# Kernel optimization log

Measured on AMD Instinct MI355X. Metric: run time of the kernel, lower is better.

The kernel has to match this reference:

```python
import math
import jax, jax.numpy as jnp
import numpy as np

MUL = 8      # multiplicity of 0e and 1o in irreps_in/out
KS = 5       # kernel spatial extent (diameter 5, steps 1 -> coords -2..2)
NB = 5       # num_radial_basis
RAD = 2.5    # diameter / 2


def _sus(t):
    # e3nn sus(x) = exp(-1/x) for x>0 else 0
    return jnp.where(t > 0.0, jnp.exp(-1.0 / jnp.where(t > 0.0, t, 1.0)), 0.0)


def _emb_sh():
    c = jnp.arange(-2.0, 3.0)
    lat = jnp.stack(jnp.meshgrid(c, c, c, indexing='ij'), axis=-1)  # (5,5,5,3)
    d = jnp.linalg.norm(lat, axis=-1)
    # soft_one_hot_linspace(basis='smooth_finite', cutoff=True)
    values = jnp.linspace(0.0, RAD, NB + 2)
    step = values[1] - values[0]
    diff = (d[..., None] - values[1:-1]) / step
    emb = 1.14136 * math.exp(2.0) * _sus(diff + 1.0) * _sus(1.0 - diff)  # (5,5,5,NB)
    # real spherical harmonics, lmax=2, normalize=True, normalization='component'
    safe = jnp.where(d > 0.0, d, 1.0)[..., None]
    u = jnp.where(d[..., None] > 0.0, lat / safe, 0.0)
    x, y, z = u[..., 0], u[..., 1], u[..., 2]
    s3, s5, s15 = math.sqrt(3.0), math.sqrt(5.0), math.sqrt(15.0)
    sh = jnp.stack([
        jnp.ones_like(x),
        s3 * x, s3 * y, s3 * z,
        s15 * x * z, s15 * x * y,
        s5 * (y * y - 0.5 * (x * x + z * z)),
        s15 * y * z, (s15 / 2.0) * (z * z - x * x),
    ], axis=-1)  # (5,5,5,9)
    return emb, sh


def _c121():
    # Clebsch-Gordan (w3j) for 1o x 2e -> 1o in the real e3nn basis, built from the
    # orthonormal symmetric-traceless matrix basis matching the l=2 SH component order.
    s2, s6 = math.sqrt(2.0), math.sqrt(6.0)
    S = np.zeros((5, 3, 3))
    S[0, 0, 2] = S[0, 2, 0] = 1.0 / s2            # xz
    S[1, 0, 1] = S[1, 1, 0] = 1.0 / s2            # xy
    S[2] = np.diag([-1.0, 2.0, -1.0]) / s6        # 2y^2 - x^2 - z^2
    S[3, 1, 2] = S[3, 2, 1] = 1.0 / s2            # yz
    S[4] = np.diag([-1.0, 0.0, 1.0]) / s2         # z^2 - x^2
    # w3j(1,2,1)[m,j,k] = S[j,m,k]/sqrt(5)  (fully symmetric since l1+l2+l3 even)
    return jnp.asarray(np.transpose(S, (1, 0, 2)) / math.sqrt(5.0), dtype=jnp.float32)


def _build_kernel(weight, emb, sh, c121, dtype):
    g = (KS, KS, KS)
    W = (emb @ weight) / float(KS * KS * KS)  # (5,5,5,320)
    w1, w2, w3, w4, w5 = [W[..., 64 * i:64 * (i + 1)].reshape(g + (MUL, MUL)) for i in range(5)]
    sh0, sh1, sh2 = sh[..., 0], sh[..., 1:4], sh[..., 4:9]
    pw0 = math.sqrt(1.0 / 16.0)   # output 0e: alpha=1, fan_in=8+8
    pw1 = math.sqrt(3.0 / 24.0)   # output 1o: alpha=3, fan_in=8+8+8
    inv_s3 = 1.0 / math.sqrt(3.0)
    K00 = pw0 * sh0[..., None, None] * w1                                   # (g,u,w)
    K01 = (pw1 * inv_s3) * jnp.einsum('xyzuw,xyzk->xyzuwk', w2, sh1)        # (g,u,w,k)
    K10 = (pw0 * inv_s3) * jnp.einsum('xyzuw,xyzm->xyzumw', w4, sh1)        # (g,u,m,w)
    T = jnp.einsum('xyzj,mjk->xyzmk', sh2, c121)                            # (g,m,k)
    eye3 = jnp.eye(3, dtype=dtype)
    K11 = pw1 * (inv_s3 * jnp.einsum('xyzuw,mk->xyzumwk', sh0[..., None, None] * w3, eye3)
                 + jnp.einsum('xyzuw,xyzmk->xyzumwk', w5, T))               # (g,u,m,w,k)
    D = 4 * MUL
    kern = jnp.zeros(g + (D, D), dtype=dtype)
    kern = kern.at[..., :MUL, :MUL].set(K00)
    kern = kern.at[..., :MUL, MUL:].set(K01.reshape(g + (MUL, 3 * MUL)))
    kern = kern.at[..., MUL:, :MUL].set(K10.reshape(g + (3 * MUL, MUL)))
    kern = kern.at[..., MUL:, MUL:].set(K11.reshape(g + (3 * MUL, 3 * MUL)))
    return jnp.transpose(kern, (4, 3, 0, 1, 2))  # 'xyzio->oixyz'


def reference(x, weight, w_sc0, w_sc1):
    emb, sh = _emb_sh()
    c121 = _c121()
    kern = _build_kernel(weight, emb, sh, c121, x.dtype)
    B, _, X, Y, Z = x.shape
    inv_s8 = 1.0 / math.sqrt(MUL)
    # self-connection: e3nn Linear, 0e->0e and 1o->1o blocks
    x0 = x[:, :MUL]
    x1 = x[:, MUL:].reshape(B, MUL, 3, X, Y, Z)
    sc0 = inv_s8 * jnp.einsum('uv,buxyz->bvxyz', w_sc0, x0)
    sc1 = inv_s8 * jnp.einsum('uv,bumxyz->bvmxyz', w_sc1, x1).reshape(B, 3 * MUL, X, Y, Z)
    sc = jnp.concatenate([sc0, sc1], axis=1)
    conv = jax.lax.conv_general_dilated(
        x, kern, window_strides=(1, 1, 1), padding=[(2, 2)] * 3,
        dimension_numbers=('NCDHW', 'OIDHW', 'NCDHW'))
    return sc + conv


def setup_inputs() -> dict:
    key = jax.random.key(0)
    k1, k2, k3, k4 = jax.random.split(key, 4)
    return {
        'x': jax.random.normal(k1, (2, 32, 64, 64, 64), dtype=jnp.float32),
        'weight': jax.random.normal(k2, (NB, 5 * MUL * MUL), dtype=jnp.float32),
        'w_sc0': jax.random.normal(k3, (MUL, MUL), dtype=jnp.float32),
        'w_sc1': jax.random.normal(k4, (MUL, MUL), dtype=jnp.float32),
    }
```

## Files before the change

### kernel.cpp

```cpp
#include <hip/hip_runtime.h>
#include <math.h>

typedef __attribute__((ext_vector_type(8))) short short8;
typedef __attribute__((ext_vector_type(4))) float f32x4;
typedef __attribute__((ext_vector_type(16))) float f32x16;

#define NTAP 125
#define DCH 32

static __device__ __forceinline__ unsigned short f2bf(float f) {
    union { float f; unsigned u; } v; v.f = f;
    unsigned u = v.u;
    return (unsigned short)((u + 0x7FFFu + ((u >> 16) & 1u)) >> 16);
}

static __device__ __forceinline__ void gld_lds16(const void* g, void* l) {
    __builtin_amdgcn_global_load_lds(
        (const __attribute__((address_space(1))) unsigned int*)g,
        (__attribute__((address_space(3))) unsigned int*)l, 16, 0, 0);
}

__global__ __launch_bounds__(128) void build_pack(
    const float* __restrict__ weight,
    const float* __restrict__ w_sc0,
    const float* __restrict__ w_sc1,
    unsigned short* __restrict__ kwb,
    float4* __restrict__ zpg)
{
    const int t = blockIdx.x;
    if (t == 0) {
        float4 z4 = make_float4(0.f, 0.f, 0.f, 0.f);
        zpg[threadIdx.x * 2] = z4;
        zpg[threadIdx.x * 2 + 1] = z4;
    }
    const int dx = t / 25, dy = (t / 5) % 5, dz = t % 5;
    const float px = dx - 2.0f, py = dy - 2.0f, pz = dz - 2.0f;
    const float d = sqrtf(px * px + py * py + pz * pz);

    const float stepv = 2.5f / 6.0f;
    const float embc = 1.14136f * expf(2.0f);
    float emb[5];
#pragma unroll
    for (int n = 0; n < 5; ++n) {
        float diff = (d - stepv * (float)(n + 1)) / stepv;
        float a = diff + 1.0f, bb = 1.0f - diff;
        float v = 0.0f;
        if (a > 0.0f && bb > 0.0f)
            v = embc * expf(-1.0f / a) * expf(-1.0f / bb);
        emb[n] = v;
    }

    const float inv_d = (d > 0.0f) ? 1.0f / d : 0.0f;
    const float ux = px * inv_d, uy = py * inv_d, uz = pz * inv_d;
    const float s3 = 1.73205081f, s5 = 2.23606798f, s15 = 3.87298335f;
    float sh[9];
    sh[0] = 1.0f;
    sh[1] = s3 * ux; sh[2] = s3 * uy; sh[3] = s3 * uz;
    sh[4] = s15 * ux * uz;
    sh[5] = s15 * ux * uy;
    sh[6] = s5 * (uy * uy - 0.5f * (ux * ux + uz * uz));
    sh[7] = s15 * uy * uz;
    sh[8] = 0.5f * s15 * (uz * uz - ux * ux);

    const float i_s2 = 0.70710678f, i_s6 = 0.40824829f, i_s5 = 0.44721360f;
    float T[3][3];
    T[0][0] = i_s5 * (-sh[6] * i_s6 - sh[8] * i_s2);
    T[0][1] = i_s5 * (sh[5] * i_s2);
    T[0][2] = i_s5 * (sh[4] * i_s2);
    T[1][0] = T[0][1];
    T[1][1] = i_s5 * (2.0f * sh[6] * i_s6);
    T[1][2] = i_s5 * (sh[7] * i_s2);
    T[2][0] = T[0][2];
    T[2][1] = T[1][2];
    T[2][2] = i_s5 * (-sh[6] * i_s6 + sh[8] * i_s2);

    __shared__ float Wt[320];
    __shared__ float kws[1024];
    for (int col = threadIdx.x; col < 320; col += 128) {
        float a = 0.0f;
#pragma unroll
        for (int n = 0; n < 5; ++n) a += emb[n] * weight[n * 320 + col];
        Wt[col] = a * (1.0f / 125.0f);
    }
    __syncthreads();

    const float pw0 = 0.25f;
    const float pw1 = 0.35355339f;
    const float inv_s3 = 0.57735027f;
    const float inv_s8 = 0.35355339f;

    for (int idx = threadIdx.x; idx < 1024; idx += 128) {
        const int o = idx >> 5, i = idx & 31;
        float val;
        if (o < 8) {
            if (i < 8) {
                val = pw0 * Wt[i * 8 + o];
            } else {
                const int u = (i - 8) / 3, m = (i - 8) % 3;
                val = pw0 * inv_s3 * Wt[192 + u * 8 + o] * sh[1 + m];
            }
        } else {
            const int v = (o - 8) / 3, k = (o - 8) % 3;
            if (i < 8) {
                val = pw1 * inv_s3 * Wt[64 + i * 8 + v] * sh[1 + k];
            } else {
                const int u = (i - 8) / 3, m = (i - 8) % 3;
                float tv = Wt[256 + u * 8 + v] * T[m][k];
                if (m == k) tv += inv_s3 * Wt[128 + u * 8 + v];
                val = pw1 * tv;
            }
        }
        if (t == 62) {
            if (o < 8 && i < 8) {
                val += inv_s8 * w_sc0[i * 8 + o];
            } else if (o >= 8 && i >= 8) {
                const int u = (i - 8) / 3, m = (i - 8) % 3;
                const int v = (o - 8) / 3, k = (o - 8) % 3;
                if (m == k) val += inv_s8 * w_sc1[u * 8 + v];
            }
        }
        kws[i * 32 + o] = val;
    }
    __syncthreads();

    const int tid = threadIdx.x;
    const int kh = tid >> 6, l = tid & 63;
    const int co = l & 31;
    const int cib = kh * 16 + (l >> 5) * 8;
    unsigned short v[8];
#pragma unroll
    for (int j = 0; j < 8; ++j)
        v[j] = f2bf(kws[(cib + j) * 32 + co]);
    uint4 o;
    o.x = (unsigned)v[0] | ((unsigned)v[1] << 16);
    o.y = (unsigned)v[2] | ((unsigned)v[3] << 16);
    o.z = (unsigned)v[4] | ((unsigned)v[5] << 16);
    o.w = (unsigned)v[6] | ((unsigned)v[7] << 16);
    *reinterpret_cast<uint4*>(kwb + ((size_t)(t * 2 + kh) * 64 + l) * 8) = o;
}

__global__ __launch_bounds__(256) void xpose(
    const float* __restrict__ x, unsigned short* __restrict__ xt)
{
    const int xx = blockIdx.x, yy = blockIdx.y, b = blockIdx.z;
    const int t = threadIdx.x;
    const int z = t & 63, part = t >> 6;
    const float* src = x + ((((size_t)b * 32) * 64 + xx) * 64 + yy) * 64 + z;
    unsigned short v[8];
#pragma unroll
    for (int j = 0; j < 8; ++j)
        v[j] = f2bf(src[(size_t)(part * 8 + j) * 262144]);
    uint4 o;
    o.x = (unsigned)v[0] | ((unsigned)v[1] << 16);
    o.y = (unsigned)v[2] | ((unsigned)v[3] << 16);
    o.z = (unsigned)v[4] | ((unsigned)v[5] << 16);
    o.w = (unsigned)v[6] | ((unsigned)v[7] << 16);
    *reinterpret_cast<uint4*>(
        xt + ((((size_t)b * 64 + xx) * 64 + yy) * 64 + z) * 32 + part * 8) = o;
}

__global__ __launch_bounds__(512, 2) void conv_mfma(
    const unsigned short* __restrict__ xt,
    const unsigned short* __restrict__ kwb,
    const unsigned short* __restrict__ zpage,
    float* __restrict__ out)
{
    extern __shared__ unsigned short smem[];
    char* lds = (char*)smem;

    const int tid = threadIdx.x;
    const int lane = tid & 63;
    const int wv = tid >> 6;
    const int oyp = wv >> 1, zh = wv & 1;
    const int x0 = blockIdx.x * 4, y0 = blockIdx.y * 8;
    const int b = blockIdx.z;
    const int l31 = lane & 31, hi = lane >> 5;

    int abase[5][2];
#pragma unroll
    for (int dz = 0; dz < 5; ++dz) {
        const int s = zh * 32 + l31 + dz;
#pragma unroll
        for (int kh = 0; kh < 2; ++kh) {
            const int cph = (kh * 2 + hi) ^ ((s >> 1) & 3);
            abase[dz][kh] =
                51200 + ((((oyp * 2 * 68 + s) << 2) | cph) << 4);
        }
    }
    const int bbase = lane * 16;

    int srow[5]; int soff[5]; bool szok[5];
#pragma unroll
    for (int p = 0; p < 5; ++p) {
        const int c = tid + p * 512;
        const int row = c / 272;
        const int rem = c - row * 272;
        const int slot = rem >> 2;
        const int clog = (rem & 3) ^ ((slot >> 1) & 3);
        const int z = slot - 2;
        srow[p] = row;
        szok[p] = ((unsigned)z < 64u);
        soff[p] = row * 2048 + z * 32 + clog * 8;
    }

    int bsrc[7];
#pragma unroll
    for (int k = 0; k < 7; ++k) {
        const int c = tid + k * 512;
        const int tp = c >> 7, rem = c & 127;
        const int dxx = tp / 5, dzz = tp - dxx * 5;
        bsrc[k] = (dxx * 25 + dzz) * 128 + rem;
    }

    auto issue_bs = [&](int dy) {
#pragma unroll
        for (int k = 0; k < 7; ++k) {
            const int c0 = wv * 64 + k * 512;
            if (c0 < 3200) {
                gld_lds16(kwb + ((size_t)(bsrc[k] + dy * 640)) * 8,
                          lds + c0 * 16);
            }
        }
    };

    auto issue_slab = [&](int dyn, int xln, int bufi) {
        const int yyb = y0 + dyn - 2;
        const int xx = x0 + xln - 2;
        const bool xok = ((unsigned)xx < 64u);
        const long long xyb =
            (long long)(b * 64 + xx) * 131072 + (long long)yyb * 2048;
        char* dst = lds + 51200 + bufi * 34816;
#pragma unroll
        for (int p = 0; p < 4; ++p) {
            const int yy = yyb + srow[p];
            const bool ok = xok && ((unsigned)yy < 64u) && szok[p];
            const unsigned short* src = ok ? (xt + xyb + soff[p]) : zpage;
            gld_lds16(src, dst + (wv * 64 + p * 512) * 16);
        }
        if (wv < 2) {
            const int yy = yyb + srow[4];
            const bool ok = xok && ((unsigned)yy < 64u) && szok[4];
            const unsigned short* src = ok ? (xt + xyb + soff[4]) : zpage;
            gld_lds16(src, dst + (wv * 64 + 2048) * 16);
        }
    };

    f32x16 acc[2][4];
#pragma unroll
    for (int oyi = 0; oyi < 2; ++oyi)
#pragma unroll
        for (int ox = 0; ox < 4; ++ox)
#pragma unroll
            for (int e = 0; e < 16; ++e) acc[oyi][ox][e] = 0.0f;

    issue_bs(0);
    issue_slab(0, 0, 0);
    __syncthreads();

    for (int dy = 0; dy < 5; ++dy) {
#pragma unroll
        for (int xl = 0; xl < 8; ++xl) {
            if (xl == 0) {
                if (dy > 0) {
                    issue_bs(dy);
                    __builtin_amdgcn_sched_barrier(0);
                    issue_slab(dy, 1, 1);
                    __builtin_amdgcn_sched_barrier(0);
                    if (wv < 2)
                        asm volatile("s_waitcnt vmcnt(5)" ::: "memory");
                    else
                        asm volatile("s_waitcnt vmcnt(4)" ::: "memory");
                    __builtin_amdgcn_s_barrier();
                    __builtin_amdgcn_sched_barrier(0);
                } else {
                    issue_slab(0, 1, 1);
                }
            } else if (!(dy == 4 && xl == 7)) {
                issue_slab(xl == 7 ? dy + 1 : dy, xl == 7 ? 0 : xl + 1,
                           (xl & 1) ^ 1);
            }

            const int boff = (xl & 1) * 34816;
#pragma unroll
            for (int dz = 0; dz < 5; ++dz) {
#pragma unroll
                for (int kh = 0; kh < 2; ++kh) {
                    const short8 a0 = *reinterpret_cast<const short8*>(
                        lds + abase[dz][kh] + boff);
                    const short8 a1 = *reinterpret_cast<const short8*>(
                        lds + abase[dz][kh] + boff + 4352);
#pragma unroll
                    for (int ox = 0; ox < 4; ++ox) {
                        const int dxv = xl - ox;
                        if (dxv < 0 || dxv > 4) continue;
                        const short8 bf = *reinterpret_cast<const short8*>(
                            lds + bbase + (((dxv * 5 + dz) * 2 + kh) << 10));
                        acc[0][ox] = __builtin_amdgcn_mfma_f32_32x32x16_bf16(
                            a0, bf, acc[0][ox], 0, 0, 0);
                        acc[1][ox] = __builtin_amdgcn_mfma_f32_32x32x16_bf16(
                            a1, bf, acc[1][ox], 0, 0, 0);
                    }
                }
            }
            __syncthreads();
        }
    }

#pragma unroll
    for (int oyi = 0; oyi < 2; ++oyi) {
        const int yy = y0 + oyp * 2 + oyi;
#pragma unroll
        for (int ox = 0; ox < 4; ++ox) {
            float* base = out +
                ((((size_t)b * 32 + l31) * 64 + (x0 + ox)) * 64 + yy) * 64 +
                zh * 32 + hi * 4;
#pragma unroll
            for (int rq = 0; rq < 4; ++rq) {
                f32x4 v = { acc[oyi][ox][rq * 4 + 0], acc[oyi][ox][rq * 4 + 1],
                            acc[oyi][ox][rq * 4 + 2], acc[oyi][ox][rq * 4 + 3] };
                *reinterpret_cast<f32x4*>(base + rq * 8) = v;
            }
        }
    }
}

extern "C" void kernel_launch(void* const* d_in, const int* in_sizes, int n_in,
                              void* d_out, int out_size, void* d_ws, size_t ws_size,
                              hipStream_t stream) {
    const float* x      = (const float*)d_in[0];
    const float* weight = (const float*)d_in[1];
    const float* w_sc0  = (const float*)d_in[2];
    const float* w_sc1  = (const float*)d_in[3];
    float* out = (float*)d_out;

    char* ws = (char*)d_ws;
    unsigned short* xt  = (unsigned short*)ws;
    unsigned short* kwb = (unsigned short*)(ws + 33554432);
    unsigned short* zpg = (unsigned short*)(ws + 33810432);

    (void)hipFuncSetAttribute((const void*)conv_mfma,
                              hipFuncAttributeMaxDynamicSharedMemorySize,
                              120832);

    hipLaunchKernelGGL(build_pack, dim3(NTAP), dim3(128), 0, stream,
                       weight, w_sc0, w_sc1, kwb, (float4*)zpg);
    hipLaunchKernelGGL(xpose, dim3(64, 64, 2), dim3(256), 0, stream, x, xt);
    hipLaunchKernelGGL(conv_mfma, dim3(16, 8, 2), dim3(512), 120832, stream,
                       xt, kwb, zpg, out);
}
```

Before: 144.1 us.

## Give each wave a private input slab and drop per-step block barriers

The transposed input now carries zero padding in z (2176 elements per row), so the conv kernel no longer needs z bounds checks. Each wave loads its own private double-buffered slab of the input rows it needs, and waits on its own loads with vmcnt instead of a __syncthreads after every x step. Block-wide barriers remain only when the shared weight (B) tile is reloaded each dy. The trade-off is more LDS, since halo rows are duplicated across waves, and more redundant global loads, in exchange for much less synchronisation.

```diff
diff --git a/kernel.cpp b/kernel.cpp
--- a/kernel.cpp
+++ b/kernel.cpp
@@ -155,14 +155,21 @@
     o.y = (unsigned)v[2] | ((unsigned)v[3] << 16);
     o.z = (unsigned)v[4] | ((unsigned)v[5] << 16);
     o.w = (unsigned)v[6] | ((unsigned)v[7] << 16);
-    *reinterpret_cast<uint4*>(
-        xt + ((((size_t)b * 64 + xx) * 64 + yy) * 64 + z) * 32 + part * 8) = o;
+    unsigned short* row =
+        xt + (((size_t)b * 64 + xx) * 64 + yy) * 2176;
+    *reinterpret_cast<uint4*>(row + (size_t)(z + 2) * 32 + part * 8) = o;
+    if (t < 16) {
+        const int zi = t >> 2;
+        const int z_idx = (zi < 2) ? zi : 64 + zi;
+        uint4 zz; zz.x = zz.y = zz.z = zz.w = 0u;
+        *reinterpret_cast<uint4*>(row + (size_t)z_idx * 32 + (t & 3) * 8) = zz;
+    }
 }
 
 __global__ __launch_bounds__(512, 2) void conv_mfma(
     const unsigned short* __restrict__ xt,
     const unsigned short* __restrict__ kwb,
-    const unsigned short* __restrict__ zpage,
+    const unsigned short* __restrict__ zpg,
     float* __restrict__ out)
 {
     extern __shared__ unsigned short smem[];
@@ -176,31 +183,30 @@
     const int b = blockIdx.z;
     const int l31 = lane & 31, hi = lane >> 5;
 
+    const int wbase = 51200 + wv * 9216;
+
     int abase[5][2];
 #pragma unroll
     for (int dz = 0; dz < 5; ++dz) {
-        const int s = zh * 32 + l31 + dz;
+        const int sl = l31 + dz;
 #pragma unroll
         for (int kh = 0; kh < 2; ++kh) {
-            const int cph = (kh * 2 + hi) ^ ((s >> 1) & 3);
-            abase[dz][kh] =
-                51200 + ((((oyp * 2 * 68 + s) << 2) | cph) << 4);
+            const int C = (kh * 2 + hi) ^ ((sl >> 1) & 3);
+            abase[dz][kh] = wbase + sl * 64 + C * 16;
         }
     }
     const int bbase = lane * 16;
 
-    int srow[5]; int soff[5]; bool szok[5];
+    int srow_[5]; int soff_[5];
 #pragma unroll
     for (int p = 0; p < 5; ++p) {
-        const int c = tid + p * 512;
-        const int row = c / 272;
-        const int rem = c - row * 272;
+        const int c = p * 64 + lane;
+        const int row = (c >= 144) ? 1 : 0;
+        const int rem = c - row * 144;
         const int slot = rem >> 2;
         const int clog = (rem & 3) ^ ((slot >> 1) & 3);
-        const int z = slot - 2;
-        srow[p] = row;
-        szok[p] = ((unsigned)z < 64u);
-        soff[p] = row * 2048 + z * 32 + clog * 8;
+        srow_[p] = row;
+        soff_[p] = (zh * 32 + slot) * 32 + clog * 8;
     }
 
     int bsrc[7];
@@ -224,24 +230,22 @@
     };
 
     auto issue_slab = [&](int dyn, int xln, int bufi) {
-        const int yyb = y0 + dyn - 2;
         const int xx = x0 + xln - 2;
         const bool xok = ((unsigned)xx < 64u);
-        const long long xyb =
-            (long long)(b * 64 + xx) * 131072 + (long long)yyb * 2048;
-        char* dst = lds + 51200 + bufi * 34816;
-#pragma unroll
-        for (int p = 0; p < 4; ++p) {
-            const int yy = yyb + srow[p];
-            const bool ok = xok && ((unsigned)yy < 64u) && szok[p];
-            const unsigned short* src = ok ? (xt + xyb + soff[p]) : zpage;
-            gld_lds16(src, dst + (wv * 64 + p * 512) * 16);
-        }
-        if (wv < 2) {
-            const int yy = yyb + srow[4];
-            const bool ok = xok && ((unsigned)yy < 64u) && szok[4];
-            const unsigned short* src = ok ? (xt + xyb + soff[4]) : zpage;
-            gld_lds16(src, dst + (wv * 64 + 2048) * 16);
+        const long long xb = (long long)(b * 64 + xx) * 64;
+        char* dst = lds + wbase + bufi * 4608;
+#pragma unroll
+        for (int p = 0; p < 5; ++p) {
+            const int yy = y0 + oyp * 2 + srow_[p] + dyn - 2;
+            const bool ok = xok && ((unsigned)yy < 64u);
+            const unsigned short* src = ok
+                ? xt + (xb + yy) * 2176 + soff_[p]
+                : zpg + lane * 8;
+            if (p < 4) {
+                gld_lds16(src, dst + p * 1024);
+            } else if (lane < 32) {
+                gld_lds16(src, dst + 4096);
+            }
         }
     };
 
@@ -253,34 +257,28 @@
 #pragma unroll
             for (int e = 0; e < 16; ++e) acc[oyi][ox][e] = 0.0f;
 
+    issue_slab(0, 0, 0);
     issue_bs(0);
-    issue_slab(0, 0, 0);
+    asm volatile("s_waitcnt vmcnt(0)" ::: "memory");
     __syncthreads();
 
     for (int dy = 0; dy < 5; ++dy) {
 #pragma unroll
         for (int xl = 0; xl < 8; ++xl) {
-            if (xl == 0) {
-                if (dy > 0) {
-                    issue_bs(dy);
-                    __builtin_amdgcn_sched_barrier(0);
-                    issue_slab(dy, 1, 1);
-                    __builtin_amdgcn_sched_barrier(0);
-                    if (wv < 2)
-                        asm volatile("s_waitcnt vmcnt(5)" ::: "memory");
-                    else
-                        asm volatile("s_waitcnt vmcnt(4)" ::: "memory");
-                    __builtin_amdgcn_s_barrier();
-                    __builtin_amdgcn_sched_barrier(0);
-                } else {
-                    issue_slab(0, 1, 1);
-                }
-            } else if (!(dy == 4 && xl == 7)) {
+            if (!(dy == 4 && xl == 7)) {
                 issue_slab(xl == 7 ? dy + 1 : dy, xl == 7 ? 0 : xl + 1,
                            (xl & 1) ^ 1);
-            }
-
-            const int boff = (xl & 1) * 34816;
+                __builtin_amdgcn_sched_barrier(0);
+                asm volatile("s_waitcnt vmcnt(5)" ::: "memory");
+            } else {
+                asm volatile("s_waitcnt vmcnt(0)" ::: "memory");
+            }
+            __builtin_amdgcn_sched_barrier(0);
+            if (xl == 0 && dy > 0) {
+                __builtin_amdgcn_s_barrier();
+            }
+
+            const int boff = (xl & 1) * 4608;
 #pragma unroll
             for (int dz = 0; dz < 5; ++dz) {
 #pragma unroll
@@ -288,7 +286,7 @@
                     const short8 a0 = *reinterpret_cast<const short8*>(
                         lds + abase[dz][kh] + boff);
                     const short8 a1 = *reinterpret_cast<const short8*>(
-                        lds + abase[dz][kh] + boff + 4352);
+                        lds + abase[dz][kh] + boff + 2304);
 #pragma unroll
                     for (int ox = 0; ox < 4; ++ox) {
                         const int dxv = xl - ox;
@@ -302,7 +300,12 @@
                     }
                 }
             }
-            __syncthreads();
+
+            if (xl == 7 && dy < 4) {
+                __builtin_amdgcn_s_barrier();
+                issue_bs(dy + 1);
+                __builtin_amdgcn_sched_barrier(0);
+            }
         }
     }
 
@@ -335,16 +338,16 @@
 
     char* ws = (char*)d_ws;
     unsigned short* xt  = (unsigned short*)ws;
-    unsigned short* kwb = (unsigned short*)(ws + 33554432);
-    unsigned short* zpg = (unsigned short*)(ws + 33810432);
+    unsigned short* kwb = (unsigned short*)(ws + 35651584);
+    unsigned short* zpg = (unsigned short*)(ws + 35907584);
 
     (void)hipFuncSetAttribute((const void*)conv_mfma,
                               hipFuncAttributeMaxDynamicSharedMemorySize,
-                              120832);
+                              124928);
 
     hipLaunchKernelGGL(build_pack, dim3(NTAP), dim3(128), 0, stream,
                        weight, w_sc0, w_sc1, kwb, (float4*)zpg);
     hipLaunchKernelGGL(xpose, dim3(64, 64, 2), dim3(256), 0, stream, x, xt);
-    hipLaunchKernelGGL(conv_mfma, dim3(16, 8, 2), dim3(512), 120832, stream,
+    hipLaunchKernelGGL(conv_mfma, dim3(16, 8, 2), dim3(512), 124928, stream,
                        xt, kwb, zpg, out);
 }
```

Measured after the change: 144.6 us. No clear change (+0.4%).
